# Kernel optimization log

Hardware: AMD Instinct MI355X
Metric: run time of the kernel (lower is better)

The kernel has to match this reference:

```python
import jax, jax.numpy as jnp
import numpy as np

IN_DIM = 128
OUT_DIM = 128
N_NODES = 50000
N_EDGES = 600000

def setup_inputs() -> dict:
    key = jax.random.key(0)
    k1, k2, k3, k4, k5, k6 = jax.random.split(key, 6)
    x = jax.random.normal(k1, (N_NODES, IN_DIM), dtype=jnp.float32)
    edge_index = jax.random.randint(k2, (2, N_EDGES), 0, N_NODES, dtype=jnp.int64)
    s = 1.0 / np.sqrt(IN_DIM)
    sg = 1.0 / np.sqrt(2 * IN_DIM)
    W = jax.random.uniform(k3, (IN_DIM, OUT_DIM), minval=-s, maxval=s, dtype=jnp.float32)
    b = jax.random.uniform(k4, (OUT_DIM,), minval=-s, maxval=s, dtype=jnp.float32)
    Wg = jax.random.uniform(k5, (2 * IN_DIM, OUT_DIM), minval=-sg, maxval=sg, dtype=jnp.float32)
    bg = jax.random.uniform(k6, (OUT_DIM,), minval=-sg, maxval=sg, dtype=jnp.float32)
    return {"x": x, "W": W, "b": b, "Wg": Wg, "bg": bg, "edge_index": edge_index}

def reference(x, W, b, Wg, bg, edge_index):
    row, col = edge_index[0], edge_index[1]
    x_row = x[row]                       # [E, D]
    x_col = x[col]                       # [E, D]
    gate_input = jnp.concatenate([x_row, x_col], axis=-1)  # [E, 2D]
    gate = jax.nn.sigmoid(gate_input @ Wg + bg)             # [E, D]
    messages = gate * (x_col @ W + b)                       # [E, D]
    out = jnp.zeros_like(x).at[row].add(messages)           # scatter-add over edges
    return out + (x @ W + b)
```

## Files before the change

kernel.cpp:

```cpp
#include <hip/hip_runtime.h>
#include <math.h>

#define N_NODES 50000
#define D 128
#define N_EDGES 600000
#define MAXDEG 64

typedef __attribute__((ext_vector_type(8))) short bf16x8;
typedef __attribute__((ext_vector_type(4))) float f32x4;

__device__ __forceinline__ ushort f32_to_bf16(float f) {
    unsigned u = __float_as_uint(f);
    unsigned r = (u + 0x7FFFu + ((u >> 16) & 1u)) >> 16;
    return (ushort)r;
}
__device__ __forceinline__ float bf16_to_f32(ushort h) {
    return __uint_as_float((unsigned)h << 16);
}
__device__ __forceinline__ float lo_bf16(unsigned u) { return __uint_as_float(u << 16); }
__device__ __forceinline__ float hi_bf16(unsigned u) { return __uint_as_float(u & 0xffff0000u); }

__global__ __launch_bounds__(64) void prep_weights(
    const float* __restrict__ W, const float* __restrict__ Wg,
    ushort* __restrict__ Bh, ushort* __restrict__ Bl, int* __restrict__ cnt)
{
    if (blockIdx.x >= 96) {
        const int base = (blockIdx.x - 96) * 1024 + threadIdx.x * 16;
        #pragma unroll
        for (int j = 0; j < 4; ++j) {
            const int i = base + j * 4;
            if (i < 50048) *(int4*)&cnt[i] = make_int4(0, 0, 0, 0);
        }
        return;
    }
    const int ct = blockIdx.x >> 2, kt = blockIdx.x & 3;
    const int lane = threadIdx.x;
    const int coln = ct * 16 + (lane & 15);
    const int mat = coln >> 7, c = coln & 127;
    const int k0 = kt * 32 + (lane >> 4) * 8;
    ushort hi8[8], lo8[8];
    #pragma unroll
    for (int j = 0; j < 8; ++j) {
        const int k = k0 + j;
        float w;
        if (mat == 0)      w = W [k * D + c];
        else if (mat == 1) w = Wg[k * D + c];
        else               w = Wg[(k + D) * D + c];
        hi8[j] = f32_to_bf16(w);
        lo8[j] = f32_to_bf16(w - bf16_to_f32(hi8[j]));
    }
    const size_t off = ((size_t)blockIdx.x * 64 + lane) * 8;
    *(bf16x8*)&Bh[off] = *(const bf16x8*)hi8;
    *(bf16x8*)&Bl[off] = *(const bf16x8*)lo8;
}

__global__ __launch_bounds__(256) void node_transform_mfma(
    const float* __restrict__ x,
    const ushort* __restrict__ Bhw, const ushort* __restrict__ Blw,
    const float* __restrict__ b, const float* __restrict__ bg,
    float* __restrict__ g1, char* __restrict__ P)
{
    __shared__ ushort a_hi[32 * D];
    const int tid = threadIdx.x;
    const int node0 = blockIdx.x * 32;

    {
        const int row = tid >> 3;
        const int col0 = (tid & 7) * 16;
        const bool valid = (node0 + row) < N_NODES;
        #pragma unroll
        for (int half = 0; half < 2; ++half) {
            const int col = col0 + half * 8;
            float v[8];
            if (valid) {
                const float4 v0 = *(const float4*)&x[(size_t)(node0 + row) * D + col];
                const float4 v1 = *(const float4*)&x[(size_t)(node0 + row) * D + col + 4];
                v[0]=v0.x; v[1]=v0.y; v[2]=v0.z; v[3]=v0.w;
                v[4]=v1.x; v[5]=v1.y; v[6]=v1.z; v[7]=v1.w;
            } else {
                #pragma unroll
                for (int j = 0; j < 8; ++j) v[j] = 0.f;
            }
            ushort hi8[8];
            #pragma unroll
            for (int j = 0; j < 8; ++j) hi8[j] = f32_to_bf16(v[j]);
            int byte = row * 256 + col * 2;
            byte ^= (row & 7) << 4;
            *(bf16x8*)((char*)a_hi + byte) = *(const bf16x8*)hi8;
        }
    }
    __syncthreads();

    const int wave = tid >> 6, lane = tid & 63;
    const int arow = lane & 15;
    const int kgrp = (lane >> 4) * 8;

    bf16x8 A[2][4];
    #pragma unroll
    for (int rt = 0; rt < 2; ++rt) {
        #pragma unroll
        for (int kt = 0; kt < 4; ++kt) {
            int byte = (rt * 16 + arow) * 256 + (kt * 32 + kgrp) * 2;
            byte ^= (arow & 7) << 4;
            A[rt][kt] = *(const bf16x8*)((const char*)a_hi + byte);
        }
    }

    #pragma unroll
    for (int ct = 0; ct < 6; ++ct) {
        const int ctg = wave * 6 + ct;
        bf16x8 Bh[4], Bl[4];
        #pragma unroll
        for (int kt = 0; kt < 4; ++kt) {
            const size_t off = ((size_t)(ctg * 4 + kt) * 64 + lane) * 8;
            Bh[kt] = *(const bf16x8*)&Bhw[off];
            Bl[kt] = *(const bf16x8*)&Blw[off];
        }

        const int mat = ctg >> 3;
        const int col = (ctg & 7) * 16 + (lane & 15);
        const float bias = (mat == 0) ? b[col] : (mat == 2 ? bg[col] : 0.f);

        #pragma unroll
        for (int rt = 0; rt < 2; ++rt) {
            f32x4 acc = {0.f, 0.f, 0.f, 0.f};
            #pragma unroll
            for (int kt = 0; kt < 4; ++kt) {
                acc = __builtin_amdgcn_mfma_f32_16x16x32_bf16(A[rt][kt], Bh[kt], acc, 0, 0, 0);
                acc = __builtin_amdgcn_mfma_f32_16x16x32_bf16(A[rt][kt], Bl[kt], acc, 0, 0, 0);
            }
            #pragma unroll
            for (int i = 0; i < 4; ++i) {
                const int node = node0 + rt * 16 + (lane >> 4) * 4 + i;
                const float val = acc[i] + bias;
                if (mat == 1) {
                    if (node < N_NODES) g1[(size_t)node * D + col] = val;
                } else {
                    const unsigned mine = f32_to_bf16(val);
                    const unsigned nbr  = (unsigned)__shfl_xor((int)mine, 1);
                    if (((lane & 1) == 0) && node < N_NODES) {
                        *(unsigned*)(P + (size_t)node * 512 + ((col >> 1) << 3)
                                       + (mat == 0 ? 4 : 0)) = mine | (nbr << 16);
                    }
                }
            }
        }
    }
}

__global__ __launch_bounds__(256) void edge_place(
    const int* __restrict__ ei, int* __restrict__ cnt, int* __restrict__ scol_p)
{
    int e = blockIdx.x * 256 + threadIdx.x;
    if (e < N_EDGES) {
        const int row = ei[e];
        const int col = ei[N_EDGES + e];
        const int r = atomicAdd(&cnt[row], 1);
        if (r < MAXDEG) scol_p[((size_t)row << 6) + r] = col;
    }
}

__global__ __launch_bounds__(256) void aggregate(
    const int* __restrict__ scol_p, const int* __restrict__ cnt,
    const char* __restrict__ P, const float* __restrict__ g1,
    float* __restrict__ out)
{
    const int lane = threadIdx.x & 63;
    int node = blockIdx.x * 4 + (threadIdx.x >> 6);
    node = __builtin_amdgcn_readfirstlane(node);
    if (node >= N_NODES) return;
    const unsigned lane8 = (unsigned)lane * 8u;

    const float2 g1v = *(const float2*)&g1[(size_t)node * D + lane * 2];
    const uint2 self = *(const uint2*)(P + ((size_t)(unsigned)node << 9) + lane8);
    float2 acc = { lo_bf16(self.y), hi_bf16(self.y) };

    const int seg = node << 6;
    int n = cnt[node];
    if (n > MAXDEG) n = MAXDEG;

#define LDP(idx) (*(const uint2*)(P + ((size_t)(unsigned)scol_p[seg + (idx)] << 9) + lane8))
#define EDGE(pv) { \
    const float za = g1v.x + lo_bf16((pv).x); \
    const float zb = g1v.y + hi_bf16((pv).x); \
    acc.x = fmaf(lo_bf16((pv).y), __builtin_amdgcn_rcpf(1.f + __expf(-za)), acc.x); \
    acc.y = fmaf(hi_bf16((pv).y), __builtin_amdgcn_rcpf(1.f + __expf(-zb)), acc.y); }

    uint2 b0, b1, b2, b3;
    if (n > 0) b0 = LDP(0);
    if (n > 1) b1 = LDP(1);
    if (n > 2) b2 = LDP(2);
    if (n > 3) b3 = LDP(3);

    int t = 0;
    for (; t + 4 <= n; t += 4) {
        uint2 c0 = b0, c1 = b1, c2 = b2, c3 = b3;
        if (t + 4 < n) b0 = LDP(t + 4);
        if (t + 5 < n) b1 = LDP(t + 5);
        if (t + 6 < n) b2 = LDP(t + 6);
        if (t + 7 < n) b3 = LDP(t + 7);
        EDGE(c0); EDGE(c1); EDGE(c2); EDGE(c3);
    }
    if (t     < n) EDGE(b0);
    if (t + 1 < n) EDGE(b1);
    if (t + 2 < n) EDGE(b2);
#undef LDP
#undef EDGE

    *(float2*)&out[(size_t)node * D + lane * 2] = acc;
}

extern "C" void kernel_launch(void* const* d_in, const int* in_sizes, int n_in,
                              void* d_out, int out_size, void* d_ws, size_t ws_size,
                              hipStream_t stream) {
    const float* x  = (const float*)d_in[0];
    const float* W  = (const float*)d_in[1];
    const float* b  = (const float*)d_in[2];
    const float* Wg = (const float*)d_in[3];
    const float* bg = (const float*)d_in[4];
    const int*   ei = (const int*)d_in[5];
    float* out = (float*)d_out;

    const size_t ND = (size_t)N_NODES * D;
    float*  g1    = (float*)d_ws;
    float*  Pf    = g1 + ND;
    ushort* Bhw   = (ushort*)(Pf + ND);
    ushort* Blw   = Bhw + 96 * 64 * 8;
    int* cnt      = (int*)(Blw + 96 * 64 * 8);
    int* scol_p   = cnt + 50048;

    prep_weights<<<145, 64, 0, stream>>>(W, Wg, Bhw, Blw, cnt);
    node_transform_mfma<<<(N_NODES + 31) / 32, 256, 0, stream>>>(
        x, Bhw, Blw, b, bg, g1, (char*)Pf);
    edge_place<<<(N_EDGES + 255) / 256, 256, 0, stream>>>(ei, cnt, scol_p);
    aggregate<<<(N_NODES + 3) / 4, 256, 0, stream>>>(
        scol_p, cnt, (const char*)Pf, g1, out);
}
```

Baseline: 120.0 us.

## Fuse edge bucketing into node transform kernel and double-buffer weight fragments

Folds the edge-placement atomics into the node-transform kernel using a grid-stride loop, which removes one kernel launch and lets the atomic traffic overlap with the MFMA work. It also double-buffers the per-column-tile weight fragment loads so the next tile's B fragments are fetched while the current tile computes. The cost is higher register pressure and extra latency at the start of each transform block.

```diff
diff --git a/kernel.cpp b/kernel.cpp
--- a/kernel.cpp
+++ b/kernel.cpp
@@ -5,6 +5,7 @@
 #define D 128
 #define N_EDGES 600000
 #define MAXDEG 64
+#define NT_GRID 1563
 
 typedef __attribute__((ext_vector_type(8))) short bf16x8;
 typedef __attribute__((ext_vector_type(4))) float f32x4;
@@ -54,15 +55,23 @@
     *(bf16x8*)&Bl[off] = *(const bf16x8*)lo8;
 }
 
-__global__ __launch_bounds__(256) void node_transform_mfma(
+__global__ __launch_bounds__(256) void transform_place(
     const float* __restrict__ x,
     const ushort* __restrict__ Bhw, const ushort* __restrict__ Blw,
     const float* __restrict__ b, const float* __restrict__ bg,
-    float* __restrict__ g1, char* __restrict__ P)
+    float* __restrict__ g1, char* __restrict__ P,
+    const int* __restrict__ ei, int* __restrict__ cnt, int* __restrict__ scol_p)
 {
     __shared__ ushort a_hi[32 * D];
     const int tid = threadIdx.x;
     const int node0 = blockIdx.x * 32;
+
+    for (int e = blockIdx.x * 256 + tid; e < N_EDGES; e += NT_GRID * 256) {
+        const int row = ei[e];
+        const int col = ei[N_EDGES + e];
+        const int r = atomicAdd(&cnt[row], 1);
+        if (r < MAXDEG) scol_p[((size_t)row << 6) + r] = col;
+    }
 
     {
         const int row = tid >> 3;
@@ -106,17 +115,27 @@
         }
     }
 
+    bf16x8 Bh[2][4], Bl[2][4];
+    #pragma unroll
+    for (int kt = 0; kt < 4; ++kt) {
+        const size_t off = ((size_t)((wave * 6) * 4 + kt) * 64 + lane) * 8;
+        Bh[0][kt] = *(const bf16x8*)&Bhw[off];
+        Bl[0][kt] = *(const bf16x8*)&Blw[off];
+    }
+
     #pragma unroll
     for (int ct = 0; ct < 6; ++ct) {
+        const int cur = ct & 1, nxt = cur ^ 1;
+        if (ct < 5) {
+            #pragma unroll
+            for (int kt = 0; kt < 4; ++kt) {
+                const size_t off = ((size_t)((wave * 6 + ct + 1) * 4 + kt) * 64 + lane) * 8;
+                Bh[nxt][kt] = *(const bf16x8*)&Bhw[off];
+                Bl[nxt][kt] = *(const bf16x8*)&Blw[off];
+            }
+        }
+
         const int ctg = wave * 6 + ct;
-        bf16x8 Bh[4], Bl[4];
-        #pragma unroll
-        for (int kt = 0; kt < 4; ++kt) {
-            const size_t off = ((size_t)(ctg * 4 + kt) * 64 + lane) * 8;
-            Bh[kt] = *(const bf16x8*)&Bhw[off];
-            Bl[kt] = *(const bf16x8*)&Blw[off];
-        }
-
         const int mat = ctg >> 3;
         const int col = (ctg & 7) * 16 + (lane & 15);
         const float bias = (mat == 0) ? b[col] : (mat == 2 ? bg[col] : 0.f);
@@ -126,8 +145,8 @@
             f32x4 acc = {0.f, 0.f, 0.f, 0.f};
             #pragma unroll
             for (int kt = 0; kt < 4; ++kt) {
-                acc = __builtin_amdgcn_mfma_f32_16x16x32_bf16(A[rt][kt], Bh[kt], acc, 0, 0, 0);
-                acc = __builtin_amdgcn_mfma_f32_16x16x32_bf16(A[rt][kt], Bl[kt], acc, 0, 0, 0);
+                acc = __builtin_amdgcn_mfma_f32_16x16x32_bf16(A[rt][kt], Bh[cur][kt], acc, 0, 0, 0);
+                acc = __builtin_amdgcn_mfma_f32_16x16x32_bf16(A[rt][kt], Bl[cur][kt], acc, 0, 0, 0);
             }
             #pragma unroll
             for (int i = 0; i < 4; ++i) {
@@ -148,18 +167,6 @@
     }
 }
 
-__global__ __launch_bounds__(256) void edge_place(
-    const int* __restrict__ ei, int* __restrict__ cnt, int* __restrict__ scol_p)
-{
-    int e = blockIdx.x * 256 + threadIdx.x;
-    if (e < N_EDGES) {
-        const int row = ei[e];
-        const int col = ei[N_EDGES + e];
-        const int r = atomicAdd(&cnt[row], 1);
-        if (r < MAXDEG) scol_p[((size_t)row << 6) + r] = col;
-    }
-}
-
 __global__ __launch_bounds__(256) void aggregate(
     const int* __restrict__ scol_p, const int* __restrict__ cnt,
     const char* __restrict__ P, const float* __restrict__ g1,
@@ -230,9 +237,8 @@
     int* scol_p   = cnt + 50048;
 
     prep_weights<<<145, 64, 0, stream>>>(W, Wg, Bhw, Blw, cnt);
-    node_transform_mfma<<<(N_NODES + 31) / 32, 256, 0, stream>>>(
-        x, Bhw, Blw, b, bg, g1, (char*)Pf);
-    edge_place<<<(N_EDGES + 255) / 256, 256, 0, stream>>>(ei, cnt, scol_p);
+    transform_place<<<NT_GRID, 256, 0, stream>>>(
+        x, Bhw, Blw, b, bg, g1, (char*)Pf, ei, cnt, scol_p);
     aggregate<<<(N_NODES + 3) / 4, 256, 0, stream>>>(
         scol_p, cnt, (const char*)Pf, g1, out);
 }
```

Result: faster. 116.7 us (-2.7%).
